# Kernel tuning notes

Measured on AMD Instinct MI355X. Metric: run time of the kernel, lower is better.

The kernel has to match this reference:

```python
import jax, jax.numpy as jnp
import numpy as np

BETA = 1.0  # inverse temperature (default of retrieve())
EPS = 1e-12  # matches torch F.normalize eps


def _l2_normalize(x):
    # torch.nn.functional.normalize(p=2, dim=-1): x / max(||x||, eps)
    n = jnp.sqrt(jnp.sum(x * x, axis=-1, keepdims=True))
    return x / jnp.maximum(n, EPS)


def setup_inputs() -> dict:
    key = jax.random.key(0)
    kq, kk = jax.random.split(key)
    N, K, D = 65536, 4096, 128
    queries = jax.random.normal(kq, (N, D), dtype=jnp.float32)
    # learnable memory keys, init_std = 0.02
    keys = jax.random.normal(kk, (K, D), dtype=jnp.float32) * 0.02
    return {"queries": queries, "keys": keys}


def reference(queries, keys):
    # normalize_keys=True, normalize_queries=True
    k_n = _l2_normalize(keys)
    q_n = _l2_normalize(queries)
    # values are TIED to the raw keys parameter (get_values returns self.keys,
    # un-normalized) — only the score-side keys are normalized.
    values = keys
    scores = BETA * jnp.einsum('nd,kd->nk', q_n, k_n)  # [N, K]
    attention = jax.nn.softmax(scores, axis=-1)
    retrieved = jnp.einsum('nk,kd->nd', attention, values)  # [N, D]
    return retrieved
```

## Files before the change

### kernel.cpp

```cpp
#include <hip/hip_runtime.h>
#include <hip/hip_bf16.h>
#include <stdint.h>


typedef __attribute__((ext_vector_type(8))) short bf16x8;
typedef __attribute__((ext_vector_type(4))) float f32x4;

#define MFMA16(a, b, c) __builtin_amdgcn_mfma_f32_16x16x32_bf16(a, b, c, 0, 0, 0)

#define ASYNC_CP16(gsrc, ldst)                                                  \
  __builtin_amdgcn_global_load_lds(                                             \
      (const __attribute__((address_space(1))) void*)(gsrc),                    \
      (__attribute__((address_space(3))) void*)(ldst), 16, 0, 0)

__device__ __forceinline__ unsigned short f2bf(float x) {
  union { float f; unsigned int u; } v; v.f = x;
  unsigned int r = v.u + 0x7fffu + ((v.u >> 16) & 1u);
  return (unsigned short)(r >> 16);
}

__global__ __launch_bounds__(256) void norm_q(const float* __restrict__ q,
                                              unsigned int* __restrict__ qn, int N) {
  const int wave = threadIdx.x >> 6, lane = threadIdx.x & 63;
  const int row = blockIdx.x * 4 + wave;
  const float2 v = ((const float2*)(q + (size_t)row * 128))[lane];
  float ss = v.x * v.x + v.y * v.y;
#pragma unroll
  for (int off = 32; off; off >>= 1) ss += __shfl_xor(ss, off);
  const float s = ss > 0.f ? rsqrtf(ss) : 0.f;
  const unsigned int w =
      (unsigned int)f2bf(v.x * s) | ((unsigned int)f2bf(v.y * s) << 16);
  qn[(size_t)row * 64 + lane] = w;
}

__global__ __launch_bounds__(256) void prep_k(const float* __restrict__ k,
                                              unsigned int* __restrict__ knsw,
                                              unsigned short* __restrict__ vtsw, int K) {
  const int wave = threadIdx.x >> 6, lane = threadIdx.x & 63;
  const int key = blockIdx.x * 4 + wave;
  const float2 v = ((const float2*)(k + (size_t)key * 128))[lane];
  float ss = v.x * v.x + v.y * v.y;
#pragma unroll
  for (int off = 32; off; off >>= 1) ss += __shfl_xor(ss, off);
  const float s = ss > 0.f ? rsqrtf(ss) : 0.f;
  const unsigned int w =
      (unsigned int)f2bf(v.x * s) | ((unsigned int)f2bf(v.y * s) << 16);
  const int j = lane >> 2;
  const int pj = j ^ (key & 15);
  knsw[(size_t)key * 64 + pj * 4 + (lane & 3)] = w;
  const int t = key & 63, k0 = key & ~63;
  const int d0 = 2 * lane, d1 = 2 * lane + 1;
  vtsw[(size_t)d0 * K + k0 + (((t >> 3) ^ (d0 & 7)) << 3) + (t & 7)] = f2bf(v.x);
  vtsw[(size_t)d1 * K + k0 + (((t >> 3) ^ (d1 & 7)) << 3) + (t & 7)] = f2bf(v.y);
}

__global__ __launch_bounds__(256, 2) void attn_main(
    const unsigned int* __restrict__ qn, const char* __restrict__ knsw,
    const char* __restrict__ vtsw, float* __restrict__ out, int N, int K) {
  __shared__ __align__(16) char smem[16384 + 16384 + 4 * 32 * 72 * 2];
  char* sKn = smem;
  char* sVt = smem + 16384;
  const int tid = threadIdx.x;
  const int wave = tid >> 6, lane = tid & 63;
  const int g = lane >> 4, c = lane & 15;
  char* sP = smem + 32768 + wave * 4608;
  const int rowbase = blockIdx.x * 128 + wave * 32;

  bf16x8 qf[2][4];
#pragma unroll
  for (int mb = 0; mb < 2; ++mb)
#pragma unroll
    for (int ks = 0; ks < 4; ++ks)
      qf[mb][ks] = *(const bf16x8*)((const char*)qn +
                    (size_t)(rowbase + mb * 16 + c) * 256 + ks * 64 + g * 16);

  f32x4 acc[2][8];
  float den[2][4];
#pragma unroll
  for (int mb = 0; mb < 2; ++mb) {
#pragma unroll
    for (int nb = 0; nb < 8; ++nb) acc[mb][nb] = (f32x4){0.f, 0.f, 0.f, 0.f};
#pragma unroll
    for (int r = 0; r < 4; ++r) den[mb][r] = 0.f;
  }

  const int nIter = K >> 6;
  const size_t vstride = (size_t)K * 2;

  for (int it = 0; it < nIter; ++it) {
    const int kt = it << 6;
    __syncthreads();
#pragma unroll
    for (int i = 0; i < 4; ++i)
      ASYNC_CP16(knsw + (size_t)kt * 256 + wave * 4096 + i * 1024 + lane * 16,
                 sKn + wave * 4096 + i * 1024);
#pragma unroll
    for (int i = 0; i < 4; ++i)
      ASYNC_CP16(vtsw + (size_t)(wave * 32 + i * 8 + (lane >> 3)) * vstride +
                     (size_t)kt * 2 + (lane & 7) * 16,
                 sVt + wave * 4096 + i * 1024);
    __syncthreads();

#pragma unroll
    for (int nb = 0; nb < 4; ++nb) {
      f32x4 s0 = {0.f, 0.f, 0.f, 0.f}, s1 = {0.f, 0.f, 0.f, 0.f};
#pragma unroll
      for (int ks = 0; ks < 4; ++ks) {
        const bf16x8 kf = *(const bf16x8*)(sKn + (nb * 16 + c) * 256 +
                                           (((ks * 4 + g) ^ c) << 4));
        s0 = MFMA16(qf[0][ks], kf, s0);
        s1 = MFMA16(qf[1][ks], kf, s1);
      }
#pragma unroll
      for (int r = 0; r < 4; ++r) {
        const float e0 = __builtin_amdgcn_exp2f(s0[r] * 1.44269504f);
        const float e1 = __builtin_amdgcn_exp2f(s1[r] * 1.44269504f);
        den[0][r] += e0;
        den[1][r] += e1;
        ((unsigned short*)sP)[(g * 4 + r) * 72 + nb * 16 + c] = f2bf(e0);
        ((unsigned short*)sP)[(16 + g * 4 + r) * 72 + nb * 16 + c] = f2bf(e1);
      }
    }

#pragma unroll
    for (int ks2 = 0; ks2 < 2; ++ks2) {
      const bf16x8 p0 = *(const bf16x8*)(sP + c * 144 + ks2 * 64 + g * 16);
      const bf16x8 p1 = *(const bf16x8*)(sP + (16 + c) * 144 + ks2 * 64 + g * 16);
#pragma unroll
      for (int nb = 0; nb < 8; ++nb) {
        const bf16x8 vf = *(const bf16x8*)(sVt + (nb * 16 + c) * 128 +
                                           ((((ks2 * 4 + g) ^ (c & 7))) << 4));
        acc[0][nb] = MFMA16(p0, vf, acc[0][nb]);
        acc[1][nb] = MFMA16(p1, vf, acc[1][nb]);
      }
    }
  }

#pragma unroll
  for (int mb = 0; mb < 2; ++mb)
#pragma unroll
    for (int r = 0; r < 4; ++r) {
      float d = den[mb][r];
      d += __shfl_xor(d, 1);
      d += __shfl_xor(d, 2);
      d += __shfl_xor(d, 4);
      d += __shfl_xor(d, 8);
      den[mb][r] = 1.0f / d;
    }

#pragma unroll
  for (int mb = 0; mb < 2; ++mb)
#pragma unroll
    for (int nb = 0; nb < 8; ++nb)
#pragma unroll
      for (int r = 0; r < 4; ++r)
        out[(size_t)(rowbase + mb * 16 + g * 4 + r) * 128 + nb * 16 + c] =
            acc[mb][nb][r] * den[mb][r];
}

extern "C" void kernel_launch(void* const* d_in, const int* in_sizes, int n_in,
                              void* d_out, int out_size, void* d_ws, size_t ws_size,
                              hipStream_t stream) {
  const float* q = (const float*)d_in[0];
  const float* k = (const float*)d_in[1];
  const int N = in_sizes[0] / 128;
  const int K = in_sizes[1] / 128;
  char* ws = (char*)d_ws;
  unsigned int* qn = (unsigned int*)ws;
  unsigned int* knsw = (unsigned int*)(ws + (size_t)N * 256);
  unsigned short* vtsw = (unsigned short*)(ws + (size_t)N * 256 + (size_t)K * 256);
  float* out = (float*)d_out;

  norm_q<<<dim3(N / 4), dim3(256), 0, stream>>>(q, qn, N);
  prep_k<<<dim3(K / 4), dim3(256), 0, stream>>>(k, knsw, vtsw, K);
  attn_main<<<dim3(N / 128), dim3(256), 0, stream>>>(qn, (const char*)knsw,
                                                     (const char*)vtsw, out, N, K);
}
```

Before: 233.7 us.

## Rewrite attention with 32x32 MFMA, fused query norm, double-buffered keys, register-resident P

```diff
diff --git a/kernel.cpp b/kernel.cpp
--- a/kernel.cpp
+++ b/kernel.cpp
@@ -4,158 +4,206 @@
 
 
 typedef __attribute__((ext_vector_type(8))) short bf16x8;
-typedef __attribute__((ext_vector_type(4))) float f32x4;
-
-#define MFMA16(a, b, c) __builtin_amdgcn_mfma_f32_16x16x32_bf16(a, b, c, 0, 0, 0)
-
+typedef __attribute__((ext_vector_type(16))) float f32x16;
+
+#define MFMA32(a, b, c) __builtin_amdgcn_mfma_f32_32x32x16_bf16(a, b, c, 0, 0, 0)
 #define ASYNC_CP16(gsrc, ldst)                                                  \
   __builtin_amdgcn_global_load_lds(                                             \
       (const __attribute__((address_space(1))) void*)(gsrc),                    \
       (__attribute__((address_space(3))) void*)(ldst), 16, 0, 0)
 
-__device__ __forceinline__ unsigned short f2bf(float x) {
-  union { float f; unsigned int u; } v; v.f = x;
-  unsigned int r = v.u + 0x7fffu + ((v.u >> 16) & 1u);
-  return (unsigned short)(r >> 16);
-}
-
-__global__ __launch_bounds__(256) void norm_q(const float* __restrict__ q,
-                                              unsigned int* __restrict__ qn, int N) {
-  const int wave = threadIdx.x >> 6, lane = threadIdx.x & 63;
-  const int row = blockIdx.x * 4 + wave;
-  const float2 v = ((const float2*)(q + (size_t)row * 128))[lane];
-  float ss = v.x * v.x + v.y * v.y;
-#pragma unroll
-  for (int off = 32; off; off >>= 1) ss += __shfl_xor(ss, off);
-  const float s = ss > 0.f ? rsqrtf(ss) : 0.f;
-  const unsigned int w =
-      (unsigned int)f2bf(v.x * s) | ((unsigned int)f2bf(v.y * s) << 16);
-  qn[(size_t)row * 64 + lane] = w;
+__device__ __forceinline__ unsigned pkbf(float lo, float hi) {
+  union { __hip_bfloat162 h2; unsigned u; } v;
+  v.h2 = __float22bfloat162_rn(float2{lo, hi});
+  return v.u;
 }
 
 __global__ __launch_bounds__(256) void prep_k(const float* __restrict__ k,
-                                              unsigned int* __restrict__ knsw,
-                                              unsigned short* __restrict__ vtsw, int K) {
-  const int wave = threadIdx.x >> 6, lane = threadIdx.x & 63;
-  const int key = blockIdx.x * 4 + wave;
-  const float2 v = ((const float2*)(k + (size_t)key * 128))[lane];
-  float ss = v.x * v.x + v.y * v.y;
-#pragma unroll
-  for (int off = 32; off; off >>= 1) ss += __shfl_xor(ss, off);
-  const float s = ss > 0.f ? rsqrtf(ss) : 0.f;
-  const unsigned int w =
-      (unsigned int)f2bf(v.x * s) | ((unsigned int)f2bf(v.y * s) << 16);
-  const int j = lane >> 2;
-  const int pj = j ^ (key & 15);
-  knsw[(size_t)key * 64 + pj * 4 + (lane & 3)] = w;
-  const int t = key & 63, k0 = key & ~63;
-  const int d0 = 2 * lane, d1 = 2 * lane + 1;
-  vtsw[(size_t)d0 * K + k0 + (((t >> 3) ^ (d0 & 7)) << 3) + (t & 7)] = f2bf(v.x);
-  vtsw[(size_t)d1 * K + k0 + (((t >> 3) ^ (d1 & 7)) << 3) + (t & 7)] = f2bf(v.y);
+                                              char* __restrict__ knf,
+                                              char* __restrict__ vtf, int K) {
+  __shared__ float sRaw[64 * 132];
+  __shared__ float sScale[64];
+  const int tid = threadIdx.x;
+  const int kbase = blockIdx.x * 64;
+  {
+    const int key_loc = tid >> 2, dq = tid & 3;
+    const float4* src = (const float4*)(k + (size_t)(kbase + key_loc) * 128 + dq * 32);
+    float4 f[8];
+    float ss = 0.f;
+#pragma unroll
+    for (int i = 0; i < 8; ++i) {
+      f[i] = src[i];
+      ss += f[i].x * f[i].x + f[i].y * f[i].y + f[i].z * f[i].z + f[i].w * f[i].w;
+    }
+    ss += __shfl_xor(ss, 1);
+    ss += __shfl_xor(ss, 2);
+    float4* dst = (float4*)(sRaw + key_loc * 132 + dq * 32);
+#pragma unroll
+    for (int i = 0; i < 8; ++i) dst[i] = f[i];
+    if (dq == 0) sScale[key_loc] = ss > 0.f ? rsqrtf(ss) : 0.f;
+  }
+  __syncthreads();
+
+#pragma unroll
+  for (int r = 0; r < 4; ++r) {
+    const int c = r * 256 + tid;
+    const int t_loc = c >> 9, ds = (c >> 6) & 7, l = c & 63;
+    const int h5 = l >> 5, c32 = l & 31;
+    const int key_loc = t_loc * 32 + c32;
+    const float sc = sScale[key_loc];
+    const float* p = sRaw + key_loc * 132 + ds * 16 + h5 * 8;
+    uint4 w;
+    w.x = pkbf(p[0] * sc, p[1] * sc);
+    w.y = pkbf(p[2] * sc, p[3] * sc);
+    w.z = pkbf(p[4] * sc, p[5] * sc);
+    w.w = pkbf(p[6] * sc, p[7] * sc);
+    *(uint4*)(knf + ((size_t)blockIdx.x * 1024 + c) * 16) = w;
+  }
+#pragma unroll
+  for (int r = 0; r < 4; ++r) {
+    const int c = r * 256 + tid;
+    const int s = c >> 8, db2 = (c >> 6) & 3, l = c & 63;
+    const int h5 = l >> 5, c32 = l & 31;
+    const int d = db2 * 32 + c32;
+    const int kb = (s >> 1) * 32 + (s & 1) * 8 + h5 * 4;
+    float f[8];
+#pragma unroll
+    for (int j = 0; j < 8; ++j)
+      f[j] = sRaw[(kb + (j & 3) + (j >> 2) * 16) * 132 + d];
+    uint4 w;
+    w.x = pkbf(f[0], f[1]);
+    w.y = pkbf(f[2], f[3]);
+    w.z = pkbf(f[4], f[5]);
+    w.w = pkbf(f[6], f[7]);
+    *(uint4*)(vtf + ((size_t)blockIdx.x * 1024 + c) * 16) = w;
+  }
 }
 
 __global__ __launch_bounds__(256, 2) void attn_main(
-    const unsigned int* __restrict__ qn, const char* __restrict__ knsw,
-    const char* __restrict__ vtsw, float* __restrict__ out, int N, int K) {
-  __shared__ __align__(16) char smem[16384 + 16384 + 4 * 32 * 72 * 2];
-  char* sKn = smem;
-  char* sVt = smem + 16384;
+    const float* __restrict__ q, const char* __restrict__ knf,
+    const char* __restrict__ vtf, float* __restrict__ out, int K) {
+  __shared__ __align__(16) char sK[2][16384];
   const int tid = threadIdx.x;
   const int wave = tid >> 6, lane = tid & 63;
-  const int g = lane >> 4, c = lane & 15;
-  char* sP = smem + 32768 + wave * 4608;
-  const int rowbase = blockIdx.x * 128 + wave * 32;
-
-  bf16x8 qf[2][4];
-#pragma unroll
-  for (int mb = 0; mb < 2; ++mb)
-#pragma unroll
-    for (int ks = 0; ks < 4; ++ks)
-      qf[mb][ks] = *(const bf16x8*)((const char*)qn +
-                    (size_t)(rowbase + mb * 16 + c) * 256 + ks * 64 + g * 16);
-
-  f32x4 acc[2][8];
-  float den[2][4];
-#pragma unroll
-  for (int mb = 0; mb < 2; ++mb) {
-#pragma unroll
-    for (int nb = 0; nb < 8; ++nb) acc[mb][nb] = (f32x4){0.f, 0.f, 0.f, 0.f};
-#pragma unroll
-    for (int r = 0; r < 4; ++r) den[mb][r] = 0.f;
-  }
+  const int h5 = lane >> 5, c32 = lane & 31;
+  const int qrow0 = blockIdx.x * 128 + wave * 32;
+
+  bf16x8 qf[8];
+  {
+    const float* qr = q + (size_t)(qrow0 + c32) * 128;
+    float f[64];
+    float ss = 0.f;
+#pragma unroll
+    for (int ds = 0; ds < 8; ++ds) {
+      const float4 a = *(const float4*)(qr + ds * 16 + h5 * 8);
+      const float4 b = *(const float4*)(qr + ds * 16 + h5 * 8 + 4);
+      f[ds * 8 + 0] = a.x; f[ds * 8 + 1] = a.y; f[ds * 8 + 2] = a.z; f[ds * 8 + 3] = a.w;
+      f[ds * 8 + 4] = b.x; f[ds * 8 + 5] = b.y; f[ds * 8 + 6] = b.z; f[ds * 8 + 7] = b.w;
+    }
+#pragma unroll
+    for (int i = 0; i < 64; ++i) ss += f[i] * f[i];
+    ss += __shfl_xor(ss, 32);
+    const float sc = (ss > 0.f ? rsqrtf(ss) : 0.f) * 1.44269504f;
+#pragma unroll
+    for (int ds = 0; ds < 8; ++ds) {
+      union { unsigned u[4]; bf16x8 v; } t;
+#pragma unroll
+      for (int p = 0; p < 4; ++p)
+        t.u[p] = pkbf(f[ds * 8 + 2 * p] * sc, f[ds * 8 + 2 * p + 1] * sc);
+      qf[ds] = t.v;
+    }
+  }
+
+  f32x16 acc[4];
+#pragma unroll
+  for (int db2 = 0; db2 < 4; ++db2)
+#pragma unroll
+    for (int r = 0; r < 16; ++r) acc[db2][r] = 0.f;
+  float den = 0.f;
 
   const int nIter = K >> 6;
-  const size_t vstride = (size_t)K * 2;
-
+  auto stage = [&](int it, int buf) {
+#pragma unroll
+    for (int i = 0; i < 4; ++i)
+      ASYNC_CP16(knf + (size_t)it * 16384 + (wave * 4 + i) * 1024 + lane * 16,
+                 sK[buf] + (wave * 4 + i) * 1024);
+  };
+
+  stage(0, 0);
   for (int it = 0; it < nIter; ++it) {
-    const int kt = it << 6;
+    const int buf = it & 1;
     __syncthreads();
-#pragma unroll
-    for (int i = 0; i < 4; ++i)
-      ASYNC_CP16(knsw + (size_t)kt * 256 + wave * 4096 + i * 1024 + lane * 16,
-                 sKn + wave * 4096 + i * 1024);
-#pragma unroll
-    for (int i = 0; i < 4; ++i)
-      ASYNC_CP16(vtsw + (size_t)(wave * 32 + i * 8 + (lane >> 3)) * vstride +
-                     (size_t)kt * 2 + (lane & 7) * 16,
-                 sVt + wave * 4096 + i * 1024);
-    __syncthreads();
-
-#pragma unroll
-    for (int nb = 0; nb < 4; ++nb) {
-      f32x4 s0 = {0.f, 0.f, 0.f, 0.f}, s1 = {0.f, 0.f, 0.f, 0.f};
-#pragma unroll
-      for (int ks = 0; ks < 4; ++ks) {
-        const bf16x8 kf = *(const bf16x8*)(sKn + (nb * 16 + c) * 256 +
-                                           (((ks * 4 + g) ^ c) << 4));
-        s0 = MFMA16(qf[0][ks], kf, s0);
-        s1 = MFMA16(qf[1][ks], kf, s1);
+    if (it + 1 < nIter) stage(it + 1, buf ^ 1);
+
+    f32x16 S[2];
+#pragma unroll
+    for (int t = 0; t < 2; ++t) {
+      f32x16 s;
+#pragma unroll
+      for (int r = 0; r < 16; ++r) s[r] = 0.f;
+#pragma unroll
+      for (int ds = 0; ds < 8; ++ds) {
+        const bf16x8 kf = *(const bf16x8*)(sK[buf] + (t * 8 + ds) * 1024 + lane * 16);
+        s = MFMA32(kf, qf[ds], s);
       }
-#pragma unroll
-      for (int r = 0; r < 4; ++r) {
-        const float e0 = __builtin_amdgcn_exp2f(s0[r] * 1.44269504f);
-        const float e1 = __builtin_amdgcn_exp2f(s1[r] * 1.44269504f);
-        den[0][r] += e0;
-        den[1][r] += e1;
-        ((unsigned short*)sP)[(g * 4 + r) * 72 + nb * 16 + c] = f2bf(e0);
-        ((unsigned short*)sP)[(16 + g * 4 + r) * 72 + nb * 16 + c] = f2bf(e1);
+      S[t] = s;
+    }
+
+    const char* vbase = vtf + (size_t)it * 16384;
+    bf16x8 vcur[4], vnxt[4];
+#pragma unroll
+    for (int db2 = 0; db2 < 4; ++db2)
+      vcur[db2] = *(const bf16x8*)(vbase + db2 * 1024 + lane * 16);
+#pragma unroll
+    for (int s = 0; s < 4; ++s) {
+      if (s < 3)
+#pragma unroll
+        for (int db2 = 0; db2 < 4; ++db2)
+          vnxt[db2] = *(const bf16x8*)(vbase + ((s + 1) * 4 + db2) * 1024 + lane * 16);
+      const int t = s >> 1, w = s & 1;
+      float e[8];
+#pragma unroll
+      for (int j = 0; j < 8; ++j) {
+        const int rr = w * 4 + (j & 3) + (j >> 2) * 8;
+        e[j] = __builtin_amdgcn_exp2f(S[t][rr]);
       }
-    }
-
-#pragma unroll
-    for (int ks2 = 0; ks2 < 2; ++ks2) {
-      const bf16x8 p0 = *(const bf16x8*)(sP + c * 144 + ks2 * 64 + g * 16);
-      const bf16x8 p1 = *(const bf16x8*)(sP + (16 + c) * 144 + ks2 * 64 + g * 16);
-#pragma unroll
-      for (int nb = 0; nb < 8; ++nb) {
-        const bf16x8 vf = *(const bf16x8*)(sVt + (nb * 16 + c) * 128 +
-                                           ((((ks2 * 4 + g) ^ (c & 7))) << 4));
-        acc[0][nb] = MFMA16(p0, vf, acc[0][nb]);
-        acc[1][nb] = MFMA16(p1, vf, acc[1][nb]);
-      }
-    }
-  }
-
-#pragma unroll
-  for (int mb = 0; mb < 2; ++mb)
-#pragma unroll
-    for (int r = 0; r < 4; ++r) {
-      float d = den[mb][r];
-      d += __shfl_xor(d, 1);
-      d += __shfl_xor(d, 2);
-      d += __shfl_xor(d, 4);
-      d += __shfl_xor(d, 8);
-      den[mb][r] = 1.0f / d;
-    }
-
-#pragma unroll
-  for (int mb = 0; mb < 2; ++mb)
-#pragma unroll
-    for (int nb = 0; nb < 8; ++nb)
-#pragma unroll
-      for (int r = 0; r < 4; ++r)
-        out[(size_t)(rowbase + mb * 16 + g * 4 + r) * 128 + nb * 16 + c] =
-            acc[mb][nb][r] * den[mb][r];
+      den += ((e[0] + e[1]) + (e[2] + e[3])) + ((e[4] + e[5]) + (e[6] + e[7]));
+      union { unsigned u[4]; bf16x8 v; } pf;
+#pragma unroll
+      for (int j2 = 0; j2 < 4; ++j2) pf.u[j2] = pkbf(e[2 * j2], e[2 * j2 + 1]);
+#pragma unroll
+      for (int db2 = 0; db2 < 4; ++db2)
+        acc[db2] = MFMA32(vcur[db2], pf.v, acc[db2]);
+      if (s < 3)
+#pragma unroll
+        for (int db2 = 0; db2 < 4; ++db2) vcur[db2] = vnxt[db2];
+    }
+  }
+
+  den += __shfl_xor(den, 32);
+  const float rd = 1.0f / den;
+
+  __syncthreads();
+  float* wls = (float*)(&sK[0][0] + wave * 4096);
+#pragma unroll
+  for (int db2 = 0; db2 < 4; ++db2) {
+#pragma unroll
+    for (int qd = 0; qd < 4; ++qd) {
+      float4 v;
+      v.x = acc[db2][qd * 4 + 0] * rd;
+      v.y = acc[db2][qd * 4 + 1] * rd;
+      v.z = acc[db2][qd * 4 + 2] * rd;
+      v.w = acc[db2][qd * 4 + 3] * rd;
+      *(float4*)(wls + c32 * 32 + (((h5 + 2 * qd) ^ (c32 & 7)) << 2)) = v;
+    }
+#pragma unroll
+    for (int p = 0; p < 4; ++p) {
+      const int ql = p * 8 + (lane >> 3);
+      const int x = lane & 7;
+      const float4 v = *(const float4*)(wls + ql * 32 + ((x ^ (ql & 7)) << 2));
+      *(float4*)(out + (size_t)(qrow0 + ql) * 128 + db2 * 32 + x * 4) = v;
+    }
+  }
 }
 
 extern "C" void kernel_launch(void* const* d_in, const int* in_sizes, int n_in,
@@ -166,13 +214,10 @@
   const int N = in_sizes[0] / 128;
   const int K = in_sizes[1] / 128;
   char* ws = (char*)d_ws;
-  unsigned int* qn = (unsigned int*)ws;
-  unsigned int* knsw = (unsigned int*)(ws + (size_t)N * 256);
-  unsigned short* vtsw = (unsigned short*)(ws + (size_t)N * 256 + (size_t)K * 256);
+  char* knf = ws;
+  char* vtf = ws + (size_t)K * 256;
   float* out = (float*)d_out;
 
-  norm_q<<<dim3(N / 4), dim3(256), 0, stream>>>(q, qn, N);
-  prep_k<<<dim3(K / 4), dim3(256), 0, stream>>>(k, knsw, vtsw, K);
-  attn_main<<<dim3(N / 128), dim3(256), 0, stream>>>(qn, (const char*)knsw,
-                                                     (const char*)vtsw, out, N, K);
-}
+  prep_k<<<dim3(K / 64), dim3(256), 0, stream>>>(k, knf, vtf, K);
+  attn_main<<<dim3(N / 128), dim3(256), 0, stream>>>(q, knf, vtf, out, K);
+}
```

New measurement: 222.2 us. 4.9% less time.
